# Kernel tuning notes

Hardware: AMD Instinct MI355X
Metric: run time of the kernel (lower is better)

## Reference

```python
import jax, jax.numpy as jnp
import numpy as np

N = 100000   # nodes
E = 1600000  # directed edges (avg degree 16)
H = 64       # MODEL_HIDDEN_CHANNELS


def setup_inputs() -> dict:
    key = jax.random.key(0)
    ks = jax.random.split(key, 6)
    x = jax.random.normal(ks[0], (N, 1), dtype=jnp.float32)
    edge_index = jax.random.randint(ks[1], (2, E), 0, N, dtype=jnp.int32)
    w1 = jax.random.normal(ks[2], (1, H), dtype=jnp.float32) * 0.5
    b1 = jnp.zeros((H,), dtype=jnp.float32)
    w2 = jax.random.normal(ks[3], (H, H), dtype=jnp.float32) * (1.0 / np.sqrt(H))
    b2 = jnp.zeros((H,), dtype=jnp.float32)
    wfc = jax.random.normal(ks[4], (H, 1), dtype=jnp.float32) * (1.0 / np.sqrt(H))
    bfc = jnp.zeros((1,), dtype=jnp.float32)
    return {"x": x, "edge_index": edge_index, "w1": w1, "b1": b1,
            "w2": w2, "b2": b2, "wfc": wfc, "bfc": bfc}


def _gcn_conv(x, src, dst, norm, W, b, n):
    # PyG GCNConv: h = x @ W, then scatter-add of norm-weighted messages at dst, + bias
    h = x @ W                                   # [n, out]
    msg = h[src] * norm[:, None]                # gather + scale, [e, out]
    agg = jax.ops.segment_sum(msg, dst, num_segments=n)
    return agg + b


def reference(x, edge_index, w1, b1, w2, b2, wfc, bfc):
    n = x.shape[0]
    # add self-loops (PyG GCNConv default)
    loops = jnp.arange(n, dtype=edge_index.dtype)
    src = jnp.concatenate([edge_index[0], loops])
    dst = jnp.concatenate([edge_index[1], loops])
    # symmetric degree normalization D^{-1/2} A_hat D^{-1/2}
    deg = jax.ops.segment_sum(jnp.ones(src.shape[0], dtype=x.dtype), dst, num_segments=n)
    dinv = jnp.where(deg > 0, jax.lax.rsqrt(deg), 0.0)
    norm = dinv[src] * dinv[dst]
    h = jax.nn.relu(_gcn_conv(x, src, dst, norm, w1, b1, n))
    h = jax.nn.relu(_gcn_conv(h, src, dst, norm, w2, b2, n))
    out = h @ wfc + bfc                         # [n, 1]
    return out.reshape(-1)
```

## Files before the change

kernel.cpp:

```cpp
#include <hip/hip_runtime.h>


#define HCH 64
#define CHUNK 4096
#define BSH 7
#define BSZ 128
#define NBMAX 1024

__device__ __forceinline__ void lds_addf(float* p, float v) {
    __hip_atomic_fetch_add(p, v, __ATOMIC_RELAXED, __HIP_MEMORY_SCOPE_WORKGROUP);
}

__global__ __launch_bounds__(1024) void k_place(const int* __restrict__ src,
                                                const int* __restrict__ dst, int e,
                                                int nb, int cap,
                                                int* __restrict__ cursor,
                                                int* __restrict__ ov_cursor,
                                                int* __restrict__ packed,
                                                int2* __restrict__ ovbuf) {
    __shared__ int h[NBMAX];
    __shared__ int basel[NBMAX];
    __shared__ int avail[NBMAX];
    __shared__ int lpv[CHUNK];
    __shared__ short lb[CHUNK];
    int t = threadIdx.x;
    if (t < nb) h[t] = 0;
    __syncthreads();
    int cbase = blockIdx.x * CHUNK;
    int rem = min(e - cbase, CHUNK);
    int li = t * 4;
    if (li + 3 < rem) {
        int4 s4 = *(const int4*)(src + cbase + li);
        int4 d4 = *(const int4*)(dst + cbase + li);
#pragma unroll
        for (int q = 0; q < 4; q++) {
            int sv = (q == 0) ? s4.x : (q == 1) ? s4.y : (q == 2) ? s4.z : s4.w;
            int dv = (q == 0) ? d4.x : (q == 1) ? d4.y : (q == 2) ? d4.z : d4.w;
            int b = dv >> BSH;
            atomicAdd(&h[b], 1);
            lpv[li + q] = sv | ((dv & (BSZ - 1)) << 17);
            lb[li + q] = (short)b;
        }
    } else {
        for (int q = li; q < rem && q < li + 4; q++) {
            int sv = src[cbase + q], dv = dst[cbase + q];
            int b = dv >> BSH;
            atomicAdd(&h[b], 1);
            lpv[q] = sv | ((dv & (BSZ - 1)) << 17);
            lb[q] = (short)b;
        }
    }
    __syncthreads();
    if (t < nb) {
        int my = h[t];
        int av = 0, base = 0;
        if (my) {
            base = atomicAdd(&cursor[t], my);
            int room = cap - base;
            av = room < 0 ? 0 : (room > my ? my : room);
        }
        basel[t] = t * cap + base;
        avail[t] = av;
        h[t] = 0;
    }
    __syncthreads();
    int lim = min(rem, li + 4);
    for (int q = li; q < lim; q++) {
        int b = lb[q];
        int pv = lpv[q];
        int loc = atomicAdd(&h[b], 1);
        if (loc < avail[b]) {
            packed[basel[b] + loc] = pv;
        } else {
            int op = atomicAdd(ov_cursor, 1);
            ovbuf[op] = make_int2(pv & 0x1FFFF, (b << BSH) | (pv >> 17));
        }
    }
}

__global__ __launch_bounds__(512) void k_bdeg(const int* __restrict__ packed,
                                              const int* __restrict__ cursor,
                                              const int* __restrict__ ov_cursor,
                                              const int2* __restrict__ ovbuf,
                                              int cap, const float* __restrict__ x, int n,
                                              float* __restrict__ dinv,
                                              float* __restrict__ y,
                                              const float* __restrict__ w1,
                                              const float* __restrict__ b1,
                                              const float* __restrict__ w2,
                                              float* __restrict__ P) {
    __shared__ int cnt[BSZ];
    int bk = blockIdx.x, t = threadIdx.x;
    int bbase = bk * cap;
    int bcnt = min(cursor[bk], cap);
    if (t < BSZ) cnt[t] = 0;
    __syncthreads();
    for (int base = 0; base < bcnt; base += 2048) {
        int i0 = base + t * 4;
        if (i0 + 3 < bcnt) {
            int4 p = *(const int4*)(packed + bbase + i0);
            atomicAdd(&cnt[p.x >> 17], 1);
            atomicAdd(&cnt[p.y >> 17], 1);
            atomicAdd(&cnt[p.z >> 17], 1);
            atomicAdd(&cnt[p.w >> 17], 1);
        } else {
            for (int i = i0; i < bcnt && i < i0 + 4; i++)
                atomicAdd(&cnt[packed[bbase + i] >> 17], 1);
        }
    }
    int ovc = *ov_cursor;
    for (int i = t; i < ovc; i += 512) {
        int2 o = ovbuf[i];
        if ((o.y >> BSH) == bk) atomicAdd(&cnt[o.y & (BSZ - 1)], 1);
    }
    __syncthreads();
    int node = (bk << BSH) + t;
    if (t < BSZ && node < n) {
        float dv = rsqrtf((float)(cnt[t] + 1));
        dinv[node] = dv;
        y[node] = dv * x[node];
    }
    if (bk == 0 && t >= 128 && t < 384) {
        int tt = t - 128;
        int c = tt >> 6, j = tt & 63;
        float acc = 0.f;
        for (int k = 0; k < HCH; k++) {
            float w = w1[k], b = b1[k], v = w2[k * HCH + j];
            if (c == 0)      acc += (w > 0.f) ? w * v : 0.f;
            else if (c == 1) acc += (w < 0.f) ? w * v : 0.f;
            else if (c == 2) acc += (w > 0.f) ? b * v : (w == 0.f ? fmaxf(b, 0.f) * v : 0.f);
            else             acc += (w < 0.f) ? b * v : (w == 0.f ? fmaxf(b, 0.f) * v : 0.f);
        }
        P[c * HCH + j] = acc;
        if (c >= 2) {
            float f = fabsf(acc);
#pragma unroll
            for (int off = 32; off; off >>= 1) f += __shfl_xor(f, off, 64);
            if ((t & 63) == 0) atomicAdd(&P[4 * HCH], f);
        }
    }
}

__global__ __launch_bounds__(512) void k_bagg1(const int* __restrict__ packed,
                                               const int* __restrict__ cursor,
                                               const int* __restrict__ ov_cursor,
                                               const int2* __restrict__ ovbuf,
                                               int cap, const float* __restrict__ x,
                                               const float* __restrict__ dinv,
                                               const float* __restrict__ y, int n,
                                               float2* __restrict__ val2) {
    __shared__ float acc[BSZ];
    int bk = blockIdx.x, t = threadIdx.x;
    int bbase = bk * cap;
    int bcnt = min(cursor[bk], cap);
    if (t < BSZ) acc[t] = 0.f;
    __syncthreads();
    for (int base = 0; base < bcnt; base += 2048) {
        int i0 = base + t * 4;
        if (i0 + 3 < bcnt) {
            int4 p = *(const int4*)(packed + bbase + i0);
            float y0 = y[p.x & 0x1FFFF], y1 = y[p.y & 0x1FFFF];
            float y2 = y[p.z & 0x1FFFF], y3 = y[p.w & 0x1FFFF];
            lds_addf(&acc[p.x >> 17], y0);
            lds_addf(&acc[p.y >> 17], y1);
            lds_addf(&acc[p.z >> 17], y2);
            lds_addf(&acc[p.w >> 17], y3);
        } else {
            for (int i = i0; i < bcnt && i < i0 + 4; i++) {
                int p = packed[bbase + i];
                lds_addf(&acc[p >> 17], y[p & 0x1FFFF]);
            }
        }
    }
    int ovc = *ov_cursor;
    for (int i = t; i < ovc; i += 512) {
        int2 o = ovbuf[i];
        if ((o.y >> BSH) == bk) lds_addf(&acc[o.y & (BSZ - 1)], y[o.x]);
    }
    __syncthreads();
    int node = (bk << BSH) + t;
    if (t < BSZ && node < n) {
        float dv = dinv[node];
        float s = dv * (acc[t] + dv * x[node]);
        val2[node] = make_float2(dv * s, dv);
    }
}

__global__ __launch_bounds__(512) void k_bagg2(const int* __restrict__ packed,
                                               const int* __restrict__ cursor,
                                               const int* __restrict__ ov_cursor,
                                               const int2* __restrict__ ovbuf,
                                               int cap, const float2* __restrict__ val2,
                                               const float* __restrict__ dinv,
                                               const float* __restrict__ P,
                                               const float* __restrict__ b2,
                                               const float* __restrict__ wfc,
                                               const float* __restrict__ bfc,
                                               float* __restrict__ out, int n) {
    __shared__ float aa[2 * BSZ];
    __shared__ float cc[2 * BSZ];
    __shared__ float sP[4 * HCH], sb2[HCH], swfc[HCH];
    int bk = blockIdx.x, t = threadIdx.x;
    int bbase = bk * cap;
    int bcnt = min(cursor[bk], cap);
    if (t < 2 * BSZ) { aa[t] = 0.f; cc[t] = 0.f; }
    if (t < 4 * HCH) sP[t] = P[t];
    if (t >= 256 && t < 320) sb2[t - 256] = b2[t - 256];
    if (t >= 320 && t < 384) swfc[t - 320] = wfc[t - 320];
    __syncthreads();
    bool useB = P[4 * HCH] != 0.f;
    for (int base = 0; base < bcnt; base += 2048) {
        int i0 = base + t * 4;
        if (i0 + 3 < bcnt) {
            int4 p = *(const int4*)(packed + bbase + i0);
            float2 v0 = val2[p.x & 0x1FFFF], v1 = val2[p.y & 0x1FFFF];
            float2 v2 = val2[p.z & 0x1FFFF], v3 = val2[p.w & 0x1FFFF];
            int o0 = (v0.x > 0.f ? 0 : BSZ) + (p.x >> 17);
            int o1 = (v1.x > 0.f ? 0 : BSZ) + (p.y >> 17);
            int o2 = (v2.x > 0.f ? 0 : BSZ) + (p.z >> 17);
            int o3 = (v3.x > 0.f ? 0 : BSZ) + (p.w >> 17);
            lds_addf(&aa[o0], v0.x); lds_addf(&aa[o1], v1.x);
            lds_addf(&aa[o2], v2.x); lds_addf(&aa[o3], v3.x);
            if (useB) {
                lds_addf(&cc[o0], v0.y); lds_addf(&cc[o1], v1.y);
                lds_addf(&cc[o2], v2.y); lds_addf(&cc[o3], v3.y);
            }
        } else {
            for (int i = i0; i < bcnt && i < i0 + 4; i++) {
                int p = packed[bbase + i];
                float2 v = val2[p & 0x1FFFF];
                int off = (v.x > 0.f ? 0 : BSZ) + (p >> 17);
                lds_addf(&aa[off], v.x);
                if (useB) lds_addf(&cc[off], v.y);
            }
        }
    }
    int ovc = *ov_cursor;
    for (int i = t; i < ovc; i += 512) {
        int2 o = ovbuf[i];
        if ((o.y >> BSH) == bk) {
            float2 v = val2[o.x];
            int off = (v.x > 0.f ? 0 : BSZ) + (o.y & (BSZ - 1));
            lds_addf(&aa[off], v.x);
            if (useB) lds_addf(&cc[off], v.y);
        }
    }
    __syncthreads();
    int node = (bk << BSH) + t;
    if (t >= BSZ || node >= n) return;
    float a_p = aa[t], a_m = aa[BSZ + t], c_p = cc[t], c_m = cc[BSZ + t];
    float2 sv = val2[node];
    if (sv.x > 0.f) { a_p += sv.x; c_p += sv.y; }
    else            { a_m += sv.x; c_m += sv.y; }
    float dv = dinv[node];
    float acc = 0.f;
#pragma unroll 8
    for (int j = 0; j < HCH; j++) {
        float z = dv * (a_p * sP[j] + a_m * sP[HCH + j] +
                        c_p * sP[2 * HCH + j] + c_m * sP[3 * HCH + j]) + sb2[j];
        z = fmaxf(z, 0.f);
        acc += z * swfc[j];
    }
    out[node] = acc + bfc[0];
}

extern "C" void kernel_launch(void* const* d_in, const int* in_sizes, int n_in,
                              void* d_out, int out_size, void* d_ws, size_t ws_size,
                              hipStream_t stream) {
    const float* x   = (const float*)d_in[0];
    const int*   ei  = (const int*)d_in[1];
    const float* w1  = (const float*)d_in[2];
    const float* b1  = (const float*)d_in[3];
    const float* w2  = (const float*)d_in[4];
    const float* b2  = (const float*)d_in[5];
    const float* wfc = (const float*)d_in[6];
    const float* bfc = (const float*)d_in[7];
    float* out = (float*)d_out;

    const int n = in_sizes[0];
    const int e = in_sizes[1] / 2;
    const int* src = ei;
    const int* dst = ei + e;

    const int nb = (n + BSZ - 1) >> BSH;
    int avg = (e + nb - 1) / nb;
    int cap = ((avg + avg / 4 + 64) + 15) & ~15;

    auto al = [](size_t v) { return (v + 255) & ~(size_t)255; };
    char* ws = (char*)d_ws;
    size_t o = 0;
    int* cursor    = (int*)(ws + o);  o += (size_t)NBMAX * 4;
    int* ov_cursor = (int*)(ws + o);  o += 256;
    float* P       = (float*)(ws + o); o += (4 * HCH + 8) * 4;
    size_t zbytes = o;
    o = al(o);
    float* dinv  = (float*)(ws + o);  o = al(o + (size_t)n * 4);
    float* y     = (float*)(ws + o);  o = al(o + (size_t)n * 4);
    float2* val2 = (float2*)(ws + o); o = al(o + (size_t)n * 8);
    int* packed  = (int*)(ws + o);    o = al(o + (size_t)nb * cap * 4);
    int2* ovbuf  = (int2*)(ws + o);   o = al(o + (size_t)e * 8);
    (void)ws_size;

    const int nchunk = (e + CHUNK - 1) / CHUNK;

    hipMemsetAsync(ws, 0, zbytes, stream);
    k_place<<<nchunk, 1024, 0, stream>>>(src, dst, e, nb, cap, cursor, ov_cursor,
                                         packed, ovbuf);
    k_bdeg<<<nb, 512, 0, stream>>>(packed, cursor, ov_cursor, ovbuf, cap, x, n,
                                   dinv, y, w1, b1, w2, P);
    k_bagg1<<<nb, 512, 0, stream>>>(packed, cursor, ov_cursor, ovbuf, cap, x, dinv, y,
                                    n, val2);
    k_bagg2<<<nb, 512, 0, stream>>>(packed, cursor, ov_cursor, ovbuf, cap, val2, dinv,
                                    P, b2, wfc, bfc, out, n);
}
```

Measured before the change: 139.7 us.

## Double bucket size and chunk, keep placement counters in registers

Bucket size goes from 128 to 256 nodes and the placement chunk from 4096 to 8192 edges, so each of the 1024 threads now handles 8 edges. Each edge's local slot is taken from the histogram atomic during the first pass and kept in registers. This removes the LDS staging arrays, the histogram reset and the second LDS atomic pass. Bucket capacity slack is retuned, and the bucket kernels now zero every accumulator entry since 2*BSZ equals the block size. The trade-off is fewer, larger buckets, which raises per-bucket work and LDS atomic contention in the aggregation kernels.

```diff
diff --git a/kernel.cpp b/kernel.cpp
--- a/kernel.cpp
+++ b/kernel.cpp
@@ -2,10 +2,10 @@
 
 
 #define HCH 64
-#define CHUNK 4096
-#define BSH 7
-#define BSZ 128
-#define NBMAX 1024
+#define CHUNK 8192
+#define BSH 8
+#define BSZ 256
+#define NBMAX 512
 
 __device__ __forceinline__ void lds_addf(float* p, float v) {
     __hip_atomic_fetch_add(p, v, __ATOMIC_RELAXED, __HIP_MEMORY_SCOPE_WORKGROUP);
@@ -21,33 +21,45 @@
     __shared__ int h[NBMAX];
     __shared__ int basel[NBMAX];
     __shared__ int avail[NBMAX];
-    __shared__ int lpv[CHUNK];
-    __shared__ short lb[CHUNK];
     int t = threadIdx.x;
     if (t < nb) h[t] = 0;
     __syncthreads();
     int cbase = blockIdx.x * CHUNK;
     int rem = min(e - cbase, CHUNK);
-    int li = t * 4;
-    if (li + 3 < rem) {
-        int4 s4 = *(const int4*)(src + cbase + li);
-        int4 d4 = *(const int4*)(dst + cbase + li);
-#pragma unroll
-        for (int q = 0; q < 4; q++) {
-            int sv = (q == 0) ? s4.x : (q == 1) ? s4.y : (q == 2) ? s4.z : s4.w;
-            int dv = (q == 0) ? d4.x : (q == 1) ? d4.y : (q == 2) ? d4.z : d4.w;
-            int b = dv >> BSH;
-            atomicAdd(&h[b], 1);
-            lpv[li + q] = sv | ((dv & (BSZ - 1)) << 17);
-            lb[li + q] = (short)b;
-        }
-    } else {
-        for (int q = li; q < rem && q < li + 4; q++) {
-            int sv = src[cbase + q], dv = dst[cbase + q];
-            int b = dv >> BSH;
-            atomicAdd(&h[b], 1);
-            lpv[q] = sv | ((dv & (BSZ - 1)) << 17);
-            lb[q] = (short)b;
+
+    int pv[8], bb[8], lc[8];
+    bool ok[8];
+#pragma unroll
+    for (int g = 0; g < 2; g++) {
+        int i0 = g * 4096 + t * 4;
+        if (i0 + 3 < rem) {
+            int4 s4 = *(const int4*)(src + cbase + i0);
+            int4 d4 = *(const int4*)(dst + cbase + i0);
+#pragma unroll
+            for (int q = 0; q < 4; q++) {
+                int k = g * 4 + q;
+                int sv = (q == 0) ? s4.x : (q == 1) ? s4.y : (q == 2) ? s4.z : s4.w;
+                int dv = (q == 0) ? d4.x : (q == 1) ? d4.y : (q == 2) ? d4.z : d4.w;
+                int b = dv >> BSH;
+                ok[k] = true;
+                bb[k] = b;
+                pv[k] = sv | ((dv & (BSZ - 1)) << 17);
+                lc[k] = atomicAdd(&h[b], 1);
+            }
+        } else {
+#pragma unroll
+            for (int q = 0; q < 4; q++) {
+                int k = g * 4 + q;
+                int i = i0 + q;
+                ok[k] = i < rem;
+                if (ok[k]) {
+                    int sv = src[cbase + i], dv = dst[cbase + i];
+                    int b = dv >> BSH;
+                    bb[k] = b;
+                    pv[k] = sv | ((dv & (BSZ - 1)) << 17);
+                    lc[k] = atomicAdd(&h[b], 1);
+                }
+            }
         }
     }
     __syncthreads();
@@ -61,19 +73,17 @@
         }
         basel[t] = t * cap + base;
         avail[t] = av;
-        h[t] = 0;
-    }
-    __syncthreads();
-    int lim = min(rem, li + 4);
-    for (int q = li; q < lim; q++) {
-        int b = lb[q];
-        int pv = lpv[q];
-        int loc = atomicAdd(&h[b], 1);
-        if (loc < avail[b]) {
-            packed[basel[b] + loc] = pv;
+    }
+    __syncthreads();
+#pragma unroll
+    for (int k = 0; k < 8; k++) {
+        if (!ok[k]) continue;
+        int b = bb[k];
+        if (lc[k] < avail[b]) {
+            packed[basel[b] + lc[k]] = pv[k];
         } else {
             int op = atomicAdd(ov_cursor, 1);
-            ovbuf[op] = make_int2(pv & 0x1FFFF, (b << BSH) | (pv >> 17));
+            ovbuf[op] = make_int2(pv[k] & 0x1FFFF, (b << BSH) | (pv[k] >> 17));
         }
     }
 }
@@ -203,7 +213,7 @@
     int bk = blockIdx.x, t = threadIdx.x;
     int bbase = bk * cap;
     int bcnt = min(cursor[bk], cap);
-    if (t < 2 * BSZ) { aa[t] = 0.f; cc[t] = 0.f; }
+    aa[t] = 0.f; cc[t] = 0.f;
     if (t < 4 * HCH) sP[t] = P[t];
     if (t >= 256 && t < 320) sb2[t - 256] = b2[t - 256];
     if (t >= 320 && t < 384) swfc[t - 320] = wfc[t - 320];
@@ -284,7 +294,7 @@
 
     const int nb = (n + BSZ - 1) >> BSH;
     int avg = (e + nb - 1) / nb;
-    int cap = ((avg + avg / 4 + 64) + 15) & ~15;
+    int cap = ((avg + avg / 8 + 128) + 15) & ~15;
 
     auto al = [](size_t v) { return (v + 255) & ~(size_t)255; };
     char* ws = (char*)d_ws;
```

Result: no change. 138.2 us (-1.1%).
